# Performance work log

Hardware: AMD Instinct MI355X
Metric: run time of the kernel (lower is better)

Reference implementation:

```python
import jax, jax.numpy as jnp
import numpy as np

B, N_PER, D_IN, D_OUT, E_PER = 64, 256, 256, 128, 8192  # graphs, nodes/graph, in feat, out feat (=clusters K), edges/graph
EPS = 1e-12


def _sage(h, src, dst, W, b):
    # DenseSAGEConv (mean aggregator): h [n,Din], src/dst [E]
    agg = jnp.zeros_like(h).at[dst].add(h[src])                 # sum of in-neighbor messages
    deg = jnp.zeros((h.shape[0],), h.dtype).at[dst].add(1.0)
    agg = agg / jnp.maximum(deg, 1.0)[:, None]                  # mean aggregation
    z = jnp.concatenate([h, agg], axis=-1) @ W + b              # Linear(2*Din -> Dout)
    z = z / jnp.maximum(jnp.linalg.norm(z, axis=-1, keepdims=True), EPS)  # F.normalize(p=2)
    return jax.nn.relu(z)                                       # activation


def setup_inputs() -> dict:
    key = jax.random.key(0)
    ks = jax.random.split(key, 5)
    h = jax.random.normal(ks[0], (B, N_PER, D_IN), jnp.float32)
    edge_src = jax.random.randint(ks[1], (B, E_PER), 0, N_PER)
    edge_dst = jax.random.randint(ks[2], (B, E_PER), 0, N_PER)
    s = 1.0 / np.sqrt(2 * D_IN)
    W_feat = jax.random.uniform(ks[3], (2 * D_IN, D_OUT), jnp.float32, -s, s)
    b_feat = jnp.zeros((D_OUT,), jnp.float32)
    W_pool = jax.random.uniform(ks[4], (2 * D_IN, D_OUT), jnp.float32, -s, s)
    b_pool = jnp.zeros((D_OUT,), jnp.float32)
    return {"h": h, "edge_src": edge_src, "edge_dst": edge_dst,
            "W_feat": W_feat, "b_feat": b_feat, "W_pool": W_pool, "b_pool": b_pool}


def reference(h, edge_src, edge_dst, W_feat, b_feat, W_pool, b_pool):
    sage = jax.vmap(_sage, in_axes=(0, 0, 0, None, None))
    feat = sage(h, edge_src, edge_dst, W_feat, b_feat)                          # [B,n,K]
    assign = jax.nn.softmax(sage(h, edge_src, edge_dst, W_pool, b_pool), -1)    # [B,n,K]
    # h = assign^T @ feat, per graph (equivalent to block_diag(assign)^T @ stacked feat)
    h_pool = jnp.einsum('bnk,bnd->bkd', assign, feat).reshape(B * D_OUT, D_OUT)  # [B*K, Dout]
    # adj_new = S^T A S per graph; A[dst,src]=1 per edge -> sum_e outer(S[dst_e], S[src_e])
    s_dst = jnp.take_along_axis(assign, edge_dst[:, :, None], axis=1)           # [B,E,K]
    s_src = jnp.take_along_axis(assign, edge_src[:, :, None], axis=1)           # [B,E,K]
    blocks = jnp.einsum('bek,bel->bkl', s_dst, s_src)                           # [B,K,K]
    # cross-graph blocks are exactly zero in the batched graph -> block-diagonal dense adj
    adj_new = jax.scipy.linalg.block_diag(*blocks)                              # [B*K, B*K]
    return adj_new, h_pool
```

## Files before the change

### kernel.cpp

```cpp
#include <hip/hip_runtime.h>
#include <hip/hip_bf16.h>
#include <stdint.h>

#define BG 64
#define NP 256
#define DI 256
#define DO 128
#define EP 8192


__device__ __forceinline__ int ldi(const void* p, size_t i, int i64) {
  return i64 ? (int)((const long long*)p)[i] : ((const int*)p)[i];
}

__global__ __launch_bounds__(256) void k_scatter(const void* __restrict__ esrc,
                                                 const void* __restrict__ edst,
                                                 float* __restrict__ A,
                                                 float* __restrict__ deg) {
  __shared__ int cnt;
  int b = blockIdx.x, t = threadIdx.x;
  if (t == 0) cnt = 0;
  __syncthreads();
  uint32_t w = ((const uint32_t*)esrc)[2 * t + 1];
  if (w != 0) atomicAdd(&cnt, 1);
  float4* Az = (float4*)(A + (size_t)b * NP * NP);
  for (int i = t; i < NP * NP / 4; i += 256) Az[i] = make_float4(0.f, 0.f, 0.f, 0.f);
  deg[b * NP + t] = 0.f;
  __syncthreads();
  int i64 = (cnt == 0);
  const size_t base = (size_t)b * EP;
  float* Ab = A + (size_t)b * NP * NP;
  float* degb = deg + b * NP;
  for (int e = t; e < EP; e += 256) {
    int si = ldi(esrc, base + e, i64) & (NP - 1);
    int di = ldi(edst, base + e, i64) & (NP - 1);
    atomicAdd(Ab + (size_t)di * NP + si, 1.0f);
    atomicAdd(degb + di, 1.0f);
  }
}

__global__ __launch_bounds__(256) void k_gemm_agg(const float* __restrict__ A,
                                                  const float* __restrict__ h,
                                                  const float* __restrict__ deg,
                                                  float* __restrict__ agg) {
  __shared__ __align__(16) float As[32][68];
  __shared__ __align__(16) float Hs[32][132];
  int b = blockIdx.y;
  int r0 = (blockIdx.x & 3) * 64;
  int f0 = (blockIdx.x >> 2) * 128;
  int t = threadIdx.x;
  int tr = t >> 4, tc = t & 15;
  float acc[4][8] = {};
  const float* Ab = A + (size_t)b * NP * NP;
  const float* hb = h + (size_t)b * NP * DI;
  for (int kc = 0; kc < NP; kc += 32) {
    __syncthreads();
    {
      int r = t >> 2;
      int ks = (t & 3) * 8;
      const float* src = &Ab[(size_t)(r0 + r) * NP + kc + ks];
      float4 v0 = *(const float4*)src;
      float4 v1 = *(const float4*)(src + 4);
      As[ks + 0][r] = v0.x; As[ks + 1][r] = v0.y; As[ks + 2][r] = v0.z; As[ks + 3][r] = v0.w;
      As[ks + 4][r] = v1.x; As[ks + 5][r] = v1.y; As[ks + 6][r] = v1.z; As[ks + 7][r] = v1.w;
    }
    {
      int k = t >> 3;
      int fs = (t & 7) * 16;
      const float* src = &hb[(size_t)(kc + k) * DI + f0 + fs];
#pragma unroll
      for (int j = 0; j < 4; ++j)
        *(float4*)&Hs[k][fs + j * 4] = *(const float4*)(src + j * 4);
    }
    __syncthreads();
#pragma unroll
    for (int k = 0; k < 32; ++k) {
      float a[4], ww[8];
      *(float4*)&a[0] = *(const float4*)&As[k][tr * 4];
      *(float4*)&ww[0] = *(const float4*)&Hs[k][tc * 8];
      *(float4*)&ww[4] = *(const float4*)&Hs[k][tc * 8 + 4];
#pragma unroll
      for (int i = 0; i < 4; ++i)
#pragma unroll
        for (int j = 0; j < 8; ++j)
          acc[i][j] += a[i] * ww[j];
    }
  }
#pragma unroll
  for (int i = 0; i < 4; ++i) {
    int gi = r0 + tr * 4 + i;
    float sc = 1.0f / fmaxf(deg[b * NP + gi], 1.0f);
    float* dst = &agg[((size_t)b * NP + gi) * DI + f0 + tc * 8];
    float o0[4] = { acc[i][0] * sc, acc[i][1] * sc, acc[i][2] * sc, acc[i][3] * sc };
    float o1[4] = { acc[i][4] * sc, acc[i][5] * sc, acc[i][6] * sc, acc[i][7] * sc };
    *(float4*)dst = *(float4*)o0;
    *(float4*)(dst + 4) = *(float4*)o1;
  }
}

__global__ __launch_bounds__(256) void k_gemm_zepi(const float* __restrict__ h,
                                                   const float* __restrict__ agg,
                                                   const float* __restrict__ Wf,
                                                   const float* __restrict__ Wp,
                                                   const float* __restrict__ bfe,
                                                   const float* __restrict__ bpo,
                                                   float* __restrict__ feat,
                                                   float* __restrict__ assign) {
  __shared__ __align__(16) float Xs[32][36];
  __shared__ __align__(16) float Ws[32][264];
  int r0 = blockIdx.x * 32;
  int t = threadIdx.x;
  int rg = t >> 5;
  int cg = t & 31;
  float acc[4][8] = {};
  for (int kc = 0; kc < 2 * DI; kc += 32) {
    __syncthreads();
    {
      int r = t >> 3;
      int kk = (t & 7) * 4;
      const float* src = (kc < DI) ? &h[(size_t)(r0 + r) * DI + kc + kk]
                                   : &agg[(size_t)(r0 + r) * DI + (kc - DI) + kk];
      float4 v = *(const float4*)src;
      Xs[kk + 0][r] = v.x; Xs[kk + 1][r] = v.y; Xs[kk + 2][r] = v.z; Xs[kk + 3][r] = v.w;
    }
    {
      int k = t >> 3;
      int cbase = (t & 7) * 32;
      const float* srcW = (cbase < DO) ? &Wf[(size_t)(kc + k) * DO + cbase]
                                       : &Wp[(size_t)(kc + k) * DO + cbase - DO];
#pragma unroll
      for (int j = 0; j < 8; ++j)
        *(float4*)&Ws[k][cbase + j * 4] = *(const float4*)(srcW + j * 4);
    }
    __syncthreads();
#pragma unroll
    for (int kk = 0; kk < 32; ++kk) {
      float a[4], ww[8];
      *(float4*)&a[0] = *(const float4*)&Xs[kk][rg * 4];
      *(float4*)&ww[0] = *(const float4*)&Ws[kk][cg * 8];
      *(float4*)&ww[4] = *(const float4*)&Ws[kk][cg * 8 + 4];
#pragma unroll
      for (int i = 0; i < 4; ++i)
#pragma unroll
        for (int j = 0; j < 8; ++j)
          acc[i][j] += a[i] * ww[j];
    }
  }
  int half = cg >> 4;
  float bias[8];
  {
    const float* bp = half ? bpo : bfe;
#pragma unroll
    for (int j = 0; j < 8; ++j) bias[j] = bp ? bp[(cg * 8 + j) & (DO - 1)] : 0.f;
  }
#pragma unroll
  for (int i = 0; i < 4; ++i) {
    int r = r0 + rg * 4 + i;
    float z[8];
    float ss = 0.f;
#pragma unroll
    for (int j = 0; j < 8; ++j) { z[j] = acc[i][j] + bias[j]; ss += z[j] * z[j]; }
    ss += __shfl_xor(ss, 1); ss += __shfl_xor(ss, 2);
    ss += __shfl_xor(ss, 4); ss += __shfl_xor(ss, 8);
    float inv = 1.0f / fmaxf(sqrtf(ss), 1e-12f);
    float v[8];
#pragma unroll
    for (int j = 0; j < 8; ++j) v[j] = fmaxf(z[j] * inv, 0.f);
    if (half == 0) {
      float* dst = &feat[(size_t)r * DO + cg * 8];
      *(float4*)dst = *(float4*)&v[0];
      *(float4*)(dst + 4) = *(float4*)&v[4];
    } else {
      float mx = v[0];
#pragma unroll
      for (int j = 1; j < 8; ++j) mx = fmaxf(mx, v[j]);
      mx = fmaxf(mx, __shfl_xor(mx, 1)); mx = fmaxf(mx, __shfl_xor(mx, 2));
      mx = fmaxf(mx, __shfl_xor(mx, 4)); mx = fmaxf(mx, __shfl_xor(mx, 8));
      float e[8], s = 0.f;
#pragma unroll
      for (int j = 0; j < 8; ++j) { e[j] = __expf(v[j] - mx); s += e[j]; }
      s += __shfl_xor(s, 1); s += __shfl_xor(s, 2);
      s += __shfl_xor(s, 4); s += __shfl_xor(s, 8);
      float is = 1.0f / s;
      float o[8];
#pragma unroll
      for (int j = 0; j < 8; ++j) o[j] = e[j] * is;
      float* dst = &assign[(size_t)r * DO + (cg - 16) * 8];
      *(float4*)dst = *(float4*)&o[0];
      *(float4*)(dst + 4) = *(float4*)&o[4];
    }
  }
}

__global__ __launch_bounds__(256) void k_gemm_as(const float* __restrict__ A,
                                                 const float* __restrict__ assign,
                                                 float* __restrict__ AS) {
  __shared__ __align__(16) float As[32][68];
  __shared__ __align__(16) float Bs[32][132];
  int b = blockIdx.y;
  int r0 = blockIdx.x * 64;
  int t = threadIdx.x;
  int tr = t >> 4, tc = t & 15;
  float acc[4][8] = {};
  const float* Ab = A + (size_t)b * NP * NP;
  const float* asb = assign + (size_t)b * NP * DO;
  for (int kc = 0; kc < NP; kc += 32) {
    __syncthreads();
    {
      int r = t >> 2;
      int ks = (t & 3) * 8;
      const float* src = &Ab[(size_t)(r0 + r) * NP + kc + ks];
      float4 v0 = *(const float4*)src;
      float4 v1 = *(const float4*)(src + 4);
      As[ks + 0][r] = v0.x; As[ks + 1][r] = v0.y; As[ks + 2][r] = v0.z; As[ks + 3][r] = v0.w;
      As[ks + 4][r] = v1.x; As[ks + 5][r] = v1.y; As[ks + 6][r] = v1.z; As[ks + 7][r] = v1.w;
    }
    {
      int k = t >> 3;
      int ls = (t & 7) * 16;
      const float* src = &asb[(size_t)(kc + k) * DO + ls];
#pragma unroll
      for (int j = 0; j < 4; ++j)
        *(float4*)&Bs[k][ls + j * 4] = *(const float4*)(src + j * 4);
    }
    __syncthreads();
#pragma unroll
    for (int k = 0; k < 32; ++k) {
      float a[4], ww[8];
      *(float4*)&a[0] = *(const float4*)&As[k][tr * 4];
      *(float4*)&ww[0] = *(const float4*)&Bs[k][tc * 8];
      *(float4*)&ww[4] = *(const float4*)&Bs[k][tc * 8 + 4];
#pragma unroll
      for (int i = 0; i < 4; ++i)
#pragma unroll
        for (int j = 0; j < 8; ++j)
          acc[i][j] += a[i] * ww[j];
    }
  }
#pragma unroll
  for (int i = 0; i < 4; ++i) {
    float* dst = &AS[((size_t)b * NP + r0 + tr * 4 + i) * DO + tc * 8];
    *(float4*)dst = *(float4*)&acc[i][0];
    *(float4*)(dst + 4) = *(float4*)&acc[i][4];
  }
}

__global__ __launch_bounds__(256) void k_pool(const float* __restrict__ assign,
                                              const float* __restrict__ AS,
                                              const float* __restrict__ feat,
                                              float* __restrict__ adj,
                                              float* __restrict__ hpool) {
  __shared__ __align__(16) float Ps[32][68];
  __shared__ __align__(16) float Ys[32][132];
  int b = blockIdx.y;
  int mt = blockIdx.x & 1;
  int which = blockIdx.x >> 1;
  const float* Y = which ? feat : AS;
  int m0 = mt * 64;
  int t = threadIdx.x;
  int tr = t >> 4, tc = t & 15;
  float acc[4][8] = {};
  for (int nc = 0; nc < NP; nc += 32) {
    __syncthreads();
    {
      int n = t >> 3;
      int mseg = (t & 7) * 8;
      const float* src = &assign[((size_t)b * NP + nc + n) * DO + m0 + mseg];
      *(float4*)&Ps[n][mseg] = *(const float4*)src;
      *(float4*)&Ps[n][mseg + 4] = *(const float4*)(src + 4);
    }
    {
      int n = t >> 3;
      int ds = (t & 7) * 16;
      const float* src = &Y[((size_t)b * NP + nc + n) * DO + ds];
#pragma unroll
      for (int j = 0; j < 4; ++j)
        *(float4*)&Ys[n][ds + j * 4] = *(const float4*)(src + j * 4);
    }
    __syncthreads();
#pragma unroll
    for (int n = 0; n < 32; ++n) {
      float a[4], ww[8];
      *(float4*)&a[0] = *(const float4*)&Ps[n][tr * 4];
      *(float4*)&ww[0] = *(const float4*)&Ys[n][tc * 8];
      *(float4*)&ww[4] = *(const float4*)&Ys[n][tc * 8 + 4];
#pragma unroll
      for (int i = 0; i < 4; ++i)
#pragma unroll
        for (int j = 0; j < 8; ++j)
          acc[i][j] += a[i] * ww[j];
    }
  }
  if (which == 0) {
#pragma unroll
    for (int i = 0; i < 4; ++i) {
      float* dst = &adj[(size_t)(b * DO + m0 + tr * 4 + i) * (BG * DO) + b * DO + tc * 8];
      *(float4*)dst = *(float4*)&acc[i][0];
      *(float4*)(dst + 4) = *(float4*)&acc[i][4];
    }
  } else {
#pragma unroll
    for (int i = 0; i < 4; ++i) {
      float* dst = &hpool[((size_t)b * DO + m0 + tr * 4 + i) * DO + tc * 8];
      *(float4*)dst = *(float4*)&acc[i][0];
      *(float4*)(dst + 4) = *(float4*)&acc[i][4];
    }
  }
}

extern "C" void kernel_launch(void* const* d_in, const int* in_sizes, int n_in,
                              void* d_out, int out_size, void* d_ws, size_t ws_size,
                              hipStream_t stream) {
  (void)out_size; (void)ws_size;
  int ih = -1, ie[2] = {-1, -1}, iw[2] = {-1, -1}, ib[2] = {-1, -1};
  int ne = 0, nw = 0, nb = 0;
  for (int i = 0; i < n_in; ++i) {
    long long s = in_sizes[i];
    if (s == (long long)BG * NP * DI) { if (ih < 0) ih = i; }
    else if (s == (long long)BG * EP && ne < 2) ie[ne++] = i;
    else if (s == (long long)2 * DI * DO && nw < 2) iw[nw++] = i;
    else if (s == (long long)DO && nb < 2) ib[nb++] = i;
  }
  if (ih < 0 || ne < 2 || nw < 2) {
    ih = 0;
    ie[0] = (n_in > 1) ? 1 : 0;  ie[1] = (n_in > 2) ? 2 : ie[0];
    iw[0] = (n_in > 3) ? 3 : 0;  iw[1] = (n_in > 5) ? 5 : iw[0];
    ib[0] = (n_in > 4) ? 4 : -1; ib[1] = (n_in > 6) ? 6 : -1;
    nb = (ib[1] >= 0) ? 2 : (ib[0] >= 0 ? 1 : 0);
  }
  const float* h    = (const float*)d_in[ih];
  const void* esrc  = d_in[ie[0]];
  const void* edst  = d_in[ie[1]];
  const float* Wf   = (const float*)d_in[iw[0]];
  const float* Wp   = (const float*)d_in[iw[1]];
  const float* bfe  = (nb >= 1) ? (const float*)d_in[ib[0]] : nullptr;
  const float* bpo  = (nb >= 2) ? (const float*)d_in[ib[1]] : nullptr;

  float* adj   = (float*)d_out;
  float* hpool = (float*)d_out + (size_t)(BG * DO) * (BG * DO);
  const size_t ADJ_BYTES = (size_t)(BG * DO) * (BG * DO) * sizeof(float);

  char* wb = (char*)d_ws;
  float* A      = (float*)wb;
  float* agg    = (float*)(wb + 16777216);
  float* feat   = (float*)(wb + 33554432);
  float* assign = (float*)(wb + 41943040);
  float* AS     = (float*)(wb + 50331648);
  float* deg    = (float*)(wb + 58720256);

  hipMemsetAsync(adj, 0, ADJ_BYTES, stream);
  k_scatter<<<BG, 256, 0, stream>>>(esrc, edst, A, deg);
  k_gemm_agg<<<dim3(8, BG), 256, 0, stream>>>(A, h, deg, agg);
  k_gemm_zepi<<<BG * NP / 32, 256, 0, stream>>>(h, agg, Wf, Wp, bfe, bpo, feat, assign);
  k_gemm_as<<<dim3(4, BG), 256, 0, stream>>>(A, assign, AS);
  k_pool<<<dim3(4, BG), 256, 0, stream>>>(assign, AS, feat, adj, hpool);
}
```

Measured before the change: 508.0 us.

## Fold adj zeroing into scatter kernel, use shared-memory degrees, halve gemm_as tile

Replaces the separate hipMemsetAsync of the 256MB adj output with 1024 extra blocks in the scatter kernel that write zeros, so the zeroing runs alongside the edge scatter. Degree counts are now accumulated with shared-memory atomics and written out once, avoiding global atomics on deg. The A·S GEMM uses 32-row tiles instead of 64, doubling its grid to improve occupancy at the cost of more reloads of the assign matrix. The scatter blocks now share the GPU with the heavy zeroing blocks, which may delay them.

Result: no change. 515.8 us (+1.5%).

```diff
diff --git a/kernel.cpp b/kernel.cpp
--- a/kernel.cpp
+++ b/kernel.cpp
@@ -16,27 +16,39 @@
 __global__ __launch_bounds__(256) void k_scatter(const void* __restrict__ esrc,
                                                  const void* __restrict__ edst,
                                                  float* __restrict__ A,
-                                                 float* __restrict__ deg) {
+                                                 float* __restrict__ deg,
+                                                 float* __restrict__ adj) {
+  int t = threadIdx.x;
+  if (blockIdx.x >= BG) {
+    int zb = blockIdx.x - BG;
+    float4* base = (float4*)adj + (size_t)zb * 16384;
+    const float4 z4 = make_float4(0.f, 0.f, 0.f, 0.f);
+#pragma unroll
+    for (int i = 0; i < 64; ++i) base[(size_t)i * 256 + t] = z4;
+    return;
+  }
   __shared__ int cnt;
-  int b = blockIdx.x, t = threadIdx.x;
+  __shared__ float sdeg[NP];
+  int b = blockIdx.x;
   if (t == 0) cnt = 0;
+  sdeg[t] = 0.f;
   __syncthreads();
   uint32_t w = ((const uint32_t*)esrc)[2 * t + 1];
   if (w != 0) atomicAdd(&cnt, 1);
   float4* Az = (float4*)(A + (size_t)b * NP * NP);
   for (int i = t; i < NP * NP / 4; i += 256) Az[i] = make_float4(0.f, 0.f, 0.f, 0.f);
-  deg[b * NP + t] = 0.f;
   __syncthreads();
   int i64 = (cnt == 0);
   const size_t base = (size_t)b * EP;
   float* Ab = A + (size_t)b * NP * NP;
-  float* degb = deg + b * NP;
   for (int e = t; e < EP; e += 256) {
     int si = ldi(esrc, base + e, i64) & (NP - 1);
     int di = ldi(edst, base + e, i64) & (NP - 1);
     atomicAdd(Ab + (size_t)di * NP + si, 1.0f);
-    atomicAdd(degb + di, 1.0f);
-  }
+    atomicAdd(&sdeg[di], 1.0f);
+  }
+  __syncthreads();
+  deg[b * NP + t] = sdeg[t];
 }
 
 __global__ __launch_bounds__(256) void k_gemm_agg(const float* __restrict__ A,
@@ -195,25 +207,22 @@
 __global__ __launch_bounds__(256) void k_gemm_as(const float* __restrict__ A,
                                                  const float* __restrict__ assign,
                                                  float* __restrict__ AS) {
-  __shared__ __align__(16) float As[32][68];
+  __shared__ __align__(16) float As[32][36];
   __shared__ __align__(16) float Bs[32][132];
   int b = blockIdx.y;
-  int r0 = blockIdx.x * 64;
+  int r0 = blockIdx.x * 32;
   int t = threadIdx.x;
   int tr = t >> 4, tc = t & 15;
-  float acc[4][8] = {};
+  float acc[2][8] = {};
   const float* Ab = A + (size_t)b * NP * NP;
   const float* asb = assign + (size_t)b * NP * DO;
   for (int kc = 0; kc < NP; kc += 32) {
     __syncthreads();
     {
-      int r = t >> 2;
-      int ks = (t & 3) * 8;
-      const float* src = &Ab[(size_t)(r0 + r) * NP + kc + ks];
-      float4 v0 = *(const float4*)src;
-      float4 v1 = *(const float4*)(src + 4);
-      As[ks + 0][r] = v0.x; As[ks + 1][r] = v0.y; As[ks + 2][r] = v0.z; As[ks + 3][r] = v0.w;
-      As[ks + 4][r] = v1.x; As[ks + 5][r] = v1.y; As[ks + 6][r] = v1.z; As[ks + 7][r] = v1.w;
+      int r = t >> 3;
+      int ks = (t & 7) * 4;
+      float4 v = *(const float4*)&Ab[(size_t)(r0 + r) * NP + kc + ks];
+      As[ks + 0][r] = v.x; As[ks + 1][r] = v.y; As[ks + 2][r] = v.z; As[ks + 3][r] = v.w;
     }
     {
       int k = t >> 3;
@@ -226,20 +235,17 @@
     __syncthreads();
 #pragma unroll
     for (int k = 0; k < 32; ++k) {
-      float a[4], ww[8];
-      *(float4*)&a[0] = *(const float4*)&As[k][tr * 4];
+      float a0 = As[k][tr * 2], a1 = As[k][tr * 2 + 1];
+      float ww[8];
       *(float4*)&ww[0] = *(const float4*)&Bs[k][tc * 8];
       *(float4*)&ww[4] = *(const float4*)&Bs[k][tc * 8 + 4];
 #pragma unroll
-      for (int i = 0; i < 4; ++i)
-#pragma unroll
-        for (int j = 0; j < 8; ++j)
-          acc[i][j] += a[i] * ww[j];
-    }
-  }
-#pragma unroll
-  for (int i = 0; i < 4; ++i) {
-    float* dst = &AS[((size_t)b * NP + r0 + tr * 4 + i) * DO + tc * 8];
+      for (int j = 0; j < 8; ++j) { acc[0][j] += a0 * ww[j]; acc[1][j] += a1 * ww[j]; }
+    }
+  }
+#pragma unroll
+  for (int i = 0; i < 2; ++i) {
+    float* dst = &AS[((size_t)b * NP + r0 + tr * 2 + i) * DO + tc * 8];
     *(float4*)dst = *(float4*)&acc[i][0];
     *(float4*)(dst + 4) = *(float4*)&acc[i][4];
   }
@@ -338,7 +344,6 @@
 
   float* adj   = (float*)d_out;
   float* hpool = (float*)d_out + (size_t)(BG * DO) * (BG * DO);
-  const size_t ADJ_BYTES = (size_t)(BG * DO) * (BG * DO) * sizeof(float);
 
   char* wb = (char*)d_ws;
   float* A      = (float*)wb;
@@ -348,10 +353,9 @@
   float* AS     = (float*)(wb + 50331648);
   float* deg    = (float*)(wb + 58720256);
 
-  hipMemsetAsync(adj, 0, ADJ_BYTES, stream);
-  k_scatter<<<BG, 256, 0, stream>>>(esrc, edst, A, deg);
+  k_scatter<<<BG + 1024, 256, 0, stream>>>(esrc, edst, A, deg, adj);
   k_gemm_agg<<<dim3(8, BG), 256, 0, stream>>>(A, h, deg, agg);
   k_gemm_zepi<<<BG * NP / 32, 256, 0, stream>>>(h, agg, Wf, Wp, bfe, bpo, feat, assign);
-  k_gemm_as<<<dim3(4, BG), 256, 0, stream>>>(A, assign, AS);
+  k_gemm_as<<<dim3(8, BG), 256, 0, stream>>>(A, assign, AS);
   k_pool<<<dim3(4, BG), 256, 0, stream>>>(assign, AS, feat, adj, hpool);
 }
```

## Use bf16 MFMA for the fused SAGE linear layer with pre-transposed weights

Applied to the files above, without the earlier changes.

Replaces the fp32 FMA GEMM in the feature/pool linear layer with bf16 MFMA 16x16x32 instructions. A new kernel converts and transposes both weight matrices to bf16 once per call, and activations are rounded to bf16 when staged in shared memory. This targets the scalar FMA compute cost of the 16384x512x256 GEMM but loses precision from bf16 inputs. It also launches one more kernel, removes the __launch_bounds__ from the scatter kernel, and stores outputs with less coalesced scalar writes.

Result: faster. 474.1 us (-6.7%).

```diff
diff --git a/kernel.cpp b/kernel.cpp
--- a/kernel.cpp
+++ b/kernel.cpp
@@ -9,14 +9,21 @@
 #define EP 8192
 
 
+typedef __attribute__((ext_vector_type(8))) short short8;
+typedef __attribute__((ext_vector_type(4))) float float4v;
+
 __device__ __forceinline__ int ldi(const void* p, size_t i, int i64) {
   return i64 ? (int)((const long long*)p)[i] : ((const int*)p)[i];
 }
 
-__global__ __launch_bounds__(256) void k_scatter(const void* __restrict__ esrc,
-                                                 const void* __restrict__ edst,
-                                                 float* __restrict__ A,
-                                                 float* __restrict__ deg) {
+__device__ __forceinline__ short f2b(float x) {
+  union { float f; unsigned u; } c; c.f = x;
+  unsigned r = c.u + 0x7FFFu + ((c.u >> 16) & 1u);
+  return (short)(r >> 16);
+}
+
+__global__ void k_scatter(const void* __restrict__ esrc, const void* __restrict__ edst,
+                          float* __restrict__ A, float* __restrict__ deg) {
   __shared__ int cnt;
   int b = blockIdx.x, t = threadIdx.x;
   if (t == 0) cnt = 0;
@@ -39,6 +46,32 @@
   }
 }
 
+__global__ __launch_bounds__(256) void k_wt(const float* __restrict__ Wf,
+                                            const float* __restrict__ Wp,
+                                            short* __restrict__ Wt) {
+  __shared__ __align__(16) float T[32][132];
+  int b = blockIdx.x;
+  int head = b >> 4;
+  int k0 = (b & 15) * 32;
+  const float* W = head ? Wp : Wf;
+  int t = threadIdx.x;
+  {
+    int k = t >> 3, fs = (t & 7) * 16;
+    const float* src = &W[(size_t)(k0 + k) * DO + fs];
+#pragma unroll
+    for (int j = 0; j < 4; ++j)
+      *(float4*)&T[k][fs + j * 4] = *(const float4*)(src + j * 4);
+  }
+  __syncthreads();
+  int f = t & 127, kh = (t >> 7) * 16;
+  __align__(16) short tmp[16];
+#pragma unroll
+  for (int i = 0; i < 16; ++i) tmp[i] = f2b(T[kh + i][f]);
+  short* dst = &Wt[((size_t)head * DO + f) * 512 + k0 + kh];
+  *(short8*)dst = *(short8*)&tmp[0];
+  *(short8*)(dst + 8) = *(short8*)&tmp[8];
+}
+
 __global__ __launch_bounds__(256) void k_gemm_agg(const float* __restrict__ A,
                                                   const float* __restrict__ h,
                                                   const float* __restrict__ deg,
@@ -98,96 +131,77 @@
   }
 }
 
-__global__ __launch_bounds__(256) void k_gemm_zepi(const float* __restrict__ h,
+__global__ __launch_bounds__(256) void k_zepi_mfma(const float* __restrict__ h,
                                                    const float* __restrict__ agg,
-                                                   const float* __restrict__ Wf,
-                                                   const float* __restrict__ Wp,
+                                                   const short* __restrict__ Wt,
                                                    const float* __restrict__ bfe,
                                                    const float* __restrict__ bpo,
                                                    float* __restrict__ feat,
                                                    float* __restrict__ assign) {
-  __shared__ __align__(16) float Xs[32][36];
-  __shared__ __align__(16) float Ws[32][264];
+  __shared__ __align__(16) short Xs[32][40];
   int r0 = blockIdx.x * 32;
   int t = threadIdx.x;
-  int rg = t >> 5;
-  int cg = t & 31;
-  float acc[4][8] = {};
+  int wave = t >> 6, lane = t & 63;
+  int rt = wave & 1, ch = wave >> 1;
+  int m = lane & 15, q = lane >> 4;
+  float4v acc[8];
+#pragma unroll
+  for (int i = 0; i < 8; ++i) acc[i] = (float4v){0.f, 0.f, 0.f, 0.f};
+
   for (int kc = 0; kc < 2 * DI; kc += 32) {
     __syncthreads();
     {
-      int r = t >> 3;
-      int kk = (t & 7) * 4;
-      const float* src = (kc < DI) ? &h[(size_t)(r0 + r) * DI + kc + kk]
-                                   : &agg[(size_t)(r0 + r) * DI + (kc - DI) + kk];
+      int r = t >> 3, k4 = (t & 7) * 4;
+      const float* src = (kc < DI) ? &h[(size_t)(r0 + r) * DI + kc + k4]
+                                   : &agg[(size_t)(r0 + r) * DI + (kc - DI) + k4];
       float4 v = *(const float4*)src;
-      Xs[kk + 0][r] = v.x; Xs[kk + 1][r] = v.y; Xs[kk + 2][r] = v.z; Xs[kk + 3][r] = v.w;
-    }
-    {
-      int k = t >> 3;
-      int cbase = (t & 7) * 32;
-      const float* srcW = (cbase < DO) ? &Wf[(size_t)(kc + k) * DO + cbase]
-                                       : &Wp[(size_t)(kc + k) * DO + cbase - DO];
-#pragma unroll
-      for (int j = 0; j < 8; ++j)
-        *(float4*)&Ws[k][cbase + j * 4] = *(const float4*)(srcW + j * 4);
-    }
-    __syncthreads();
-#pragma unroll
-    for (int kk = 0; kk < 32; ++kk) {
-      float a[4], ww[8];
-      *(float4*)&a[0] = *(const float4*)&Xs[kk][rg * 4];
-      *(float4*)&ww[0] = *(const float4*)&Ws[kk][cg * 8];
-      *(float4*)&ww[4] = *(const float4*)&Ws[kk][cg * 8 + 4];
-#pragma unroll
-      for (int i = 0; i < 4; ++i)
-#pragma unroll
-        for (int j = 0; j < 8; ++j)
-          acc[i][j] += a[i] * ww[j];
-    }
-  }
-  int half = cg >> 4;
+      Xs[r][k4 + 0] = f2b(v.x); Xs[r][k4 + 1] = f2b(v.y);
+      Xs[r][k4 + 2] = f2b(v.z); Xs[r][k4 + 3] = f2b(v.w);
+    }
+    __syncthreads();
+    short8 afrag = *(const short8*)&Xs[rt * 16 + m][q * 8];
+#pragma unroll
+    for (int tt = 0; tt < 8; ++tt) {
+      int n = ch * 128 + tt * 16 + m;
+      short8 bfrag = *(const short8*)&Wt[(size_t)n * 512 + kc + q * 8];
+      acc[tt] = __builtin_amdgcn_mfma_f32_16x16x32_bf16(afrag, bfrag, acc[tt], 0, 0, 0);
+    }
+  }
+
+  const float* bp = ch ? bpo : bfe;
   float bias[8];
-  {
-    const float* bp = half ? bpo : bfe;
-#pragma unroll
-    for (int j = 0; j < 8; ++j) bias[j] = bp ? bp[(cg * 8 + j) & (DO - 1)] : 0.f;
-  }
-#pragma unroll
-  for (int i = 0; i < 4; ++i) {
-    int r = r0 + rg * 4 + i;
+#pragma unroll
+  for (int tt = 0; tt < 8; ++tt) bias[tt] = bp ? bp[tt * 16 + m] : 0.f;
+#pragma unroll
+  for (int reg = 0; reg < 4; ++reg) {
+    int row = r0 + rt * 16 + q * 4 + reg;
     float z[8];
     float ss = 0.f;
 #pragma unroll
-    for (int j = 0; j < 8; ++j) { z[j] = acc[i][j] + bias[j]; ss += z[j] * z[j]; }
+    for (int tt = 0; tt < 8; ++tt) { z[tt] = acc[tt][reg] + bias[tt]; ss += z[tt] * z[tt]; }
     ss += __shfl_xor(ss, 1); ss += __shfl_xor(ss, 2);
     ss += __shfl_xor(ss, 4); ss += __shfl_xor(ss, 8);
     float inv = 1.0f / fmaxf(sqrtf(ss), 1e-12f);
     float v[8];
 #pragma unroll
-    for (int j = 0; j < 8; ++j) v[j] = fmaxf(z[j] * inv, 0.f);
-    if (half == 0) {
-      float* dst = &feat[(size_t)r * DO + cg * 8];
-      *(float4*)dst = *(float4*)&v[0];
-      *(float4*)(dst + 4) = *(float4*)&v[4];
+    for (int tt = 0; tt < 8; ++tt) v[tt] = fmaxf(z[tt] * inv, 0.f);
+    if (ch == 0) {
+#pragma unroll
+      for (int tt = 0; tt < 8; ++tt) feat[(size_t)row * DO + tt * 16 + m] = v[tt];
     } else {
       float mx = v[0];
 #pragma unroll
-      for (int j = 1; j < 8; ++j) mx = fmaxf(mx, v[j]);
+      for (int tt = 1; tt < 8; ++tt) mx = fmaxf(mx, v[tt]);
       mx = fmaxf(mx, __shfl_xor(mx, 1)); mx = fmaxf(mx, __shfl_xor(mx, 2));
       mx = fmaxf(mx, __shfl_xor(mx, 4)); mx = fmaxf(mx, __shfl_xor(mx, 8));
       float e[8], s = 0.f;
 #pragma unroll
-      for (int j = 0; j < 8; ++j) { e[j] = __expf(v[j] - mx); s += e[j]; }
+      for (int tt = 0; tt < 8; ++tt) { e[tt] = __expf(v[tt] - mx); s += e[tt]; }
       s += __shfl_xor(s, 1); s += __shfl_xor(s, 2);
       s += __shfl_xor(s, 4); s += __shfl_xor(s, 8);
       float is = 1.0f / s;
-      float o[8];
-#pragma unroll
-      for (int j = 0; j < 8; ++j) o[j] = e[j] * is;
-      float* dst = &assign[(size_t)r * DO + (cg - 16) * 8];
-      *(float4*)dst = *(float4*)&o[0];
-      *(float4*)(dst + 4) = *(float4*)&o[4];
+#pragma unroll
+      for (int tt = 0; tt < 8; ++tt) assign[(size_t)row * DO + tt * 16 + m] = e[tt] * is;
     }
   }
 }
@@ -347,11 +361,13 @@
   float* assign = (float*)(wb + 41943040);
   float* AS     = (float*)(wb + 50331648);
   float* deg    = (float*)(wb + 58720256);
+  short* Wt     = (short*)(wb + 58720256 + 65536);
 
   hipMemsetAsync(adj, 0, ADJ_BYTES, stream);
+  k_wt<<<32, 256, 0, stream>>>(Wf, Wp, Wt);
   k_scatter<<<BG, 256, 0, stream>>>(esrc, edst, A, deg);
   k_gemm_agg<<<dim3(8, BG), 256, 0, stream>>>(A, h, deg, agg);
-  k_gemm_zepi<<<BG * NP / 32, 256, 0, stream>>>(h, agg, Wf, Wp, bfe, bpo, feat, assign);
+  k_zepi_mfma<<<BG * NP / 32, 256, 0, stream>>>(h, agg, Wt, bfe, bpo, feat, assign);
   k_gemm_as<<<dim3(4, BG), 256, 0, stream>>>(A, assign, AS);
   k_pool<<<dim3(4, BG), 256, 0, stream>>>(assign, AS, feat, adj, hpool);
 }
```
